# Kernel tuning notes

Measured on AMD Instinct MI355X. Metric: run time of the kernel, lower is better.

Reference implementation:

```python
import jax, jax.numpy as jnp
import numpy as np

EPS = 1e-6
OMEGA = 0.1


def setup_inputs() -> dict:
    key = jax.random.key(0)
    k1, k2 = jax.random.split(key)
    n, d, kk = 4096, 128, 4
    inputs = jax.random.uniform(k1, (n, d), dtype=jnp.float32)  # positive so log(sim) is finite
    labels = jax.random.randint(k2, (n, kk), 0, 64, dtype=jnp.int64)
    return {"inputs": inputs, "labels": labels}


def reference(inputs, labels):
    n, kk = labels.shape
    sim = inputs @ inputs.T                      # [n, n]
    logsim = jnp.log(sim + EPS)                  # a_{jk} = log(sim[j,k]+eps)
    targets = labels[:, 0]
    eye = jnp.eye(n, dtype=bool)
    # pos_mask[j,k] = (targets[j] == targets[k]) xor diagonal
    pos = (targets[:, None] == targets[None, :]) & ~eye
    # eq[j,l,i] = (labels[l,i] == targets[j])
    eq = targets[:, None, None] == labels[None, :, :]
    m_idx = jnp.arange(kk)
    cols = kk - 1 - m_idx                        # neg_mask[m] uses label column kk-1-m
    # neg_mask[m][j,l] == 1  <=>  ~eq[j,l,kk-1-m]  AND  (m==0 or eq[j,l,kk-m])
    neq_col = ~eq[:, :, cols]                    # [j,l,m]
    prev_ok = jnp.concatenate(
        [jnp.ones((n, n, 1), dtype=bool), eq[:, :, cols[:-1]]], axis=-1)
    neg = neq_col & prev_ok                      # [j,l,m]
    # loss_pair[m] = log(Omega+eps) - log(Omega^(kk-m+1)+eps)
    lp = jnp.log(OMEGA + EPS) - jnp.log(OMEGA ** (kk - m_idx + 1) + EPS)  # [kk]
    dt = logsim.dtype
    posf = pos.astype(dt)
    negf = neg.astype(dt)
    # term = (a_jk - b_jlm)^2 with b_jlm = logsim[j,l] + 0.1*lp[m]
    # expand: sum_jklm pos*neg*(a^2 - 2ab + b^2), separable over k and (l,m)
    c = posf.sum(1)                              # [j] count of positives
    S1 = (posf * logsim).sum(1)                  # [j] sum a
    S2 = (posf * logsim ** 2).sum(1)             # [j] sum a^2
    b = logsim[:, :, None] + 0.1 * lp[None, None, :]   # [j,l,m]
    Ncnt = negf.sum(1)                           # [j,m]
    T1 = (negf * b).sum(1)                       # [j,m]
    T2 = (negf * b ** 2).sum(1)                  # [j,m]
    loss = (S2[:, None] * Ncnt - 2.0 * S1[:, None] * T1 + c[:, None] * T2).sum()
    return loss
```

## Files before the change

kernel.cpp:

```cpp
#include <hip/hip_runtime.h>
#include <math.h>

constexpr int N = 4096;
constexpr int D = 128;

constexpr size_t XBF_OFF = 0;
constexpr size_t ACC_OFF = (size_t)1 << 20;
constexpr size_t LSD_OFF = ACC_OFF + 7 * 4096 * 4;
constexpr size_t CNT_OFF = LSD_OFF + 4096 * 4;
constexpr size_t LST_OFF = CNT_OFF + 64 * 32 * 4;
constexpr size_t SUM_OFF = LST_OFF + 64 * 32 * 64 * 2;

typedef __attribute__((ext_vector_type(8))) short short8;
typedef __attribute__((ext_vector_type(4))) float floatx4;
typedef __attribute__((address_space(1))) unsigned int gu32;
typedef __attribute__((address_space(3))) unsigned int lu32;

__device__ inline unsigned f2bf(float f) {
  unsigned u = __builtin_bit_cast(unsigned, f);
  return (u + 0x7FFFu + ((u >> 16) & 1u)) >> 16;
}

__global__ __launch_bounds__(256) void k0_zero(char* __restrict__ ws, float* __restrict__ out) {
  const int idx = blockIdx.x * 256 + threadIdx.x;
  if (idx < 7 * 4096) ((float*)(ws + ACC_OFF))[idx] = 0.f;
  else ((unsigned*)(ws + CNT_OFF))[idx - 7 * 4096] = 0u;
  if (idx == 0) out[0] = 0.f;
}

__global__ __launch_bounds__(256) void k1_prep(
    const float* __restrict__ X, const int* __restrict__ labels, char* __restrict__ ws,
    float B0, float B1, float B2, float B3,
    float Q0, float Q1, float Q2, float Q3) {
  __shared__ float red[4][4];
  const int b = blockIdx.x, tid = threadIdx.x;
  if (b < 64) {
    const int t = b;
    unsigned* cnt = (unsigned*)(ws + CNT_OFF);
    unsigned short* lst = (unsigned short*)(ws + LST_OFF);
    float sg0 = 0.f, sgB = 0.f, sgQ = 0.f, ce0 = 0.f;
    for (int j = tid; j < N; j += 256) {
      const int4 L = ((const int4*)labels)[j];
      const bool e0 = (t == L.x), e1 = (t == L.y), e2 = (t == L.z), e3 = (t == L.w);
      const bool n1 = e3 && !e2, n2 = e2 && !e1, n3 = e1 && !e0;
      sg0 += (e3 ? 0.f : 1.f) + (n1 ? 1.f : 0.f) + (n2 ? 1.f : 0.f) + (n3 ? 1.f : 0.f);
      sgB += (e3 ? 0.f : B0) + (n1 ? B1 : 0.f) + (n2 ? B2 : 0.f) + (n3 ? B3 : 0.f);
      sgQ += (e3 ? 0.f : Q0) + (n1 ? Q1 : 0.f) + (n2 ? Q2 : 0.f) + (n3 ? Q3 : 0.f);
      ce0 += e0 ? 1.f : 0.f;
      const unsigned m = (e0 ? 1u : 0u) | (e1 ? 2u : 0u) | (e2 ? 4u : 0u) | (e3 ? 8u : 0u);
      if (m) {
        const int jb = j >> 7;
        const unsigned slot = atomicAdd(&cnt[t * 32 + jb], 1u);
        if (slot < 64u)
          lst[(t * 32 + jb) * 64 + slot] = (unsigned short)(((j & 127) << 4) | m);
      }
    }
    const int w = tid >> 6, lane = tid & 63;
#pragma unroll
    for (int s = 1; s <= 32; s <<= 1) {
      sg0 += __shfl_xor(sg0, s, 64); sgB += __shfl_xor(sgB, s, 64);
      sgQ += __shfl_xor(sgQ, s, 64); ce0 += __shfl_xor(ce0, s, 64);
    }
    if (lane == 0) { red[w][0] = sg0; red[w][1] = sgB; red[w][2] = sgQ; red[w][3] = ce0; }
    __syncthreads();
    if (tid == 0) {
      float* sums = (float*)(ws + SUM_OFF);
      sums[t * 4 + 0] = red[0][0] + red[1][0] + red[2][0] + red[3][0];
      sums[t * 4 + 1] = red[0][1] + red[1][1] + red[2][1] + red[3][1];
      sums[t * 4 + 2] = red[0][2] + red[1][2] + red[2][2] + red[3][2];
      sums[t * 4 + 3] = red[0][3] + red[1][3] + red[2][3] + red[3][3];
    }
  } else if (b < 320) {
    const int task = (b - 64) * 256 + tid;
    const int r   = task >> 4;
    const int blk = task & 15;
    const float4 x0 = *(const float4*)&X[r * D + blk * 8];
    const float4 x1 = *(const float4*)&X[r * D + blk * 8 + 4];
    uint4 wv;
    wv.x = f2bf(x0.x) | (f2bf(x0.y) << 16);
    wv.y = f2bf(x0.z) | (f2bf(x0.w) << 16);
    wv.z = f2bf(x1.x) | (f2bf(x1.y) << 16);
    wv.w = f2bf(x1.z) | (f2bf(x1.w) << 16);
    *(uint4*)(ws + XBF_OFF + (size_t)r * 256 + ((blk ^ (r & 15)) * 16)) = wv;
  } else {
    const int i = (b - 320) * 256 + tid;
    const float* xr = X + i * D;
    float s = 0.f;
#pragma unroll
    for (int c = 0; c < 32; ++c) {
      const float4 v = ((const float4*)xr)[c];
      s += v.x * v.x + v.y * v.y + v.z * v.z + v.w * v.w;
    }
    ((float*)(ws + LSD_OFF))[i] = __logf(s + 1e-6f);
  }
}

__global__ __launch_bounds__(512, 4) void logratio_phaseA(
    const char* __restrict__ ws_ro, const int* __restrict__ labels,
    float* acc7, float B0, float B1, float B2, float B3) {

  __shared__ __align__(16) char smem[66560];

  const int tid  = threadIdx.x;
  const int w    = tid >> 6;
  const int lane = tid & 63;
  const int lc   = lane & 15;
  const int quad = lane >> 4;
  const int jBase = blockIdx.x * 128;
  const int iBase = blockIdx.y * 128;

  const char* xbf = ws_ro + XBF_OFF;
  const char* gB_ = xbf + (size_t)jBase * 256 + w * 4096 + lane * 16;
  const char* gA_ = xbf + (size_t)iBase * 256 + w * 4096 + lane * 16;
#pragma unroll
  for (int c = 0; c < 4; ++c) {
    __builtin_amdgcn_global_load_lds((const gu32*)(gB_ + c * 1024),
                                     (lu32*)(smem + w * 4096 + c * 1024), 16, 0, 0);
    __builtin_amdgcn_global_load_lds((const gu32*)(gA_ + c * 1024),
                                     (lu32*)(smem + 32768 + w * 4096 + c * 1024), 16, 0, 0);
  }
  __syncthreads();

  floatx4 acc[8] = {};
  const char* Abase = smem + 32768 + (w * 16 + lc) * 256;
#pragma unroll
  for (int kb = 0; kb < 4; ++kb) {
    const int pb = ((kb * 4 + quad) ^ lc) * 16;
    const short8 af = *(const short8*)(Abase + pb);
    short8 bfr[8];
#pragma unroll
    for (int tn = 0; tn < 8; ++tn)
      bfr[tn] = *(const short8*)(smem + (tn * 16 + lc) * 256 + pb);
#pragma unroll
    for (int tn = 0; tn < 8; ++tn)
      acc[tn] = __builtin_amdgcn_mfma_f32_16x16x32_bf16(af, bfr[tn], acc[tn], 0, 0, 0);
  }
  __syncthreads();

  float* lsT   = (float*)smem;
  float* rowTT = (float*)(smem + 65536);

  const int r0 = w * 16 + quad * 4;
  float T0r[4] = {0.f, 0.f, 0.f, 0.f};
  float T1r[4] = {0.f, 0.f, 0.f, 0.f};
#pragma unroll
  for (int tn = 0; tn < 8; ++tn) {
    const int col = tn * 16 + lc;
    floatx4 lsv;
#pragma unroll
    for (int reg = 0; reg < 4; ++reg) {
      const float ls = __logf(acc[tn][reg] + 1e-6f);
      lsv[reg] = ls;
      T0r[reg] += ls;
      T1r[reg] = fmaf(ls, ls, T1r[reg]);
    }
    *(floatx4*)(lsT + col * 128 + (r0 ^ ((col & 7) << 2))) = lsv;
  }
#pragma unroll
  for (int reg = 0; reg < 4; ++reg) {
    float t0 = T0r[reg], t1 = T1r[reg];
#pragma unroll
    for (int s = 1; s <= 8; s <<= 1) {
      t0 += __shfl_xor(t0, s, 64);
      t1 += __shfl_xor(t1, s, 64);
    }
    if (lc == 0) {
      rowTT[(r0 + reg) * 2]     = t0;
      rowTT[(r0 + reg) * 2 + 1] = t1;
    }
  }
  __syncthreads();

  if (tid < 128) {
    const int r = tid, gi = iBase + r;
    const int t = labels[gi * 4];
    const int jb = blockIdx.x;
    const unsigned* cntA = (const unsigned*)(ws_ro + CNT_OFF);
    const unsigned short* lst = (const unsigned short*)(ws_ro + LST_OFF) + (t * 32 + jb) * 64;
    unsigned cnt = cntA[t * 32 + jb];
    if (cnt > 64u) cnt = 64u;
    float U0 = 0.f, U1 = 0.f, V = 0.f, P1 = 0.f, P2 = 0.f;
    for (unsigned k = 0; k < cnt; ++k) {
      const unsigned e = lst[k];
      const int jl = (int)(e >> 4);
      const unsigned m = e & 15u;
      const float ls = lsT[jl * 128 + (r ^ ((jl & 7) << 2))];
      const bool e0 = m & 1u, e1 = m & 2u, e2 = m & 4u, e3 = m & 8u;
      const bool n1 = e3 && !e2, n2 = e2 && !e1, n3 = e1 && !e0;
      const float dg0 = (e3 ? -1.f : 0.f) + (n1 ? 1.f : 0.f) + (n2 ? 1.f : 0.f) + (n3 ? 1.f : 0.f);
      const float dgB = (e3 ? -B0 : 0.f) + (n1 ? B1 : 0.f) + (n2 ? B2 : 0.f) + (n3 ? B3 : 0.f);
      const float e0f = e0 ? 1.f : 0.f;
      U0 = fmaf(dg0, ls, U0);
      U1 = fmaf(dg0 * ls, ls, U1);
      V  = fmaf(dgB, ls, V);
      P1 = fmaf(e0f, ls, P1);
      P2 = fmaf(e0f * ls, ls, P2);
    }
    atomicAdd(&acc7[0 * N + gi], rowTT[r * 2]);
    atomicAdd(&acc7[1 * N + gi], rowTT[r * 2 + 1]);
    atomicAdd(&acc7[2 * N + gi], U0);
    atomicAdd(&acc7[3 * N + gi], U1);
    atomicAdd(&acc7[4 * N + gi], V);
    atomicAdd(&acc7[5 * N + gi], P1);
    atomicAdd(&acc7[6 * N + gi], P2);
  }
}

__global__ __launch_bounds__(256) void logratio_phaseB(
    const char* __restrict__ ws_ro, const int* __restrict__ labels,
    float* out, float B0) {
  const int i = blockIdx.x * 256 + threadIdx.x;
  const float* acc7 = (const float*)(ws_ro + ACC_OFF);
  const float T0 = acc7[0 * N + i], T1 = acc7[1 * N + i];
  const float U0 = acc7[2 * N + i], U1 = acc7[3 * N + i];
  const float V  = acc7[4 * N + i];
  const float P1 = acc7[5 * N + i], P2 = acc7[6 * N + i];
  const int t = labels[i * 4];
  const float4 S = ((const float4*)(ws_ro + SUM_OFF))[t];
  const float lsd = ((const float*)(ws_ro + LSD_OFF))[i];
  const float c  = S.w - 1.f;
  const float S1 = P1 - lsd;
  const float S2 = P2 - lsd * lsd;
  const float A  = S.x;
  const float Bv = T0 + U0 + S.y;
  const float Cv = T1 + U1 + 2.f * fmaf(B0, T0, V) + S.z;
  float v = S2 * A - 2.f * S1 * Bv + c * Cv;
#pragma unroll
  for (int m = 32; m >= 1; m >>= 1) v += __shfl_xor(v, m, 64);
  __shared__ float wsum[4];
  if ((threadIdx.x & 63) == 0) wsum[threadIdx.x >> 6] = v;
  __syncthreads();
  if (threadIdx.x == 0) atomicAdd(out, wsum[0] + wsum[1] + wsum[2] + wsum[3]);
}

extern "C" void kernel_launch(void* const* d_in, const int* in_sizes, int n_in,
                              void* d_out, int out_size, void* d_ws, size_t ws_size,
                              hipStream_t stream) {
  const float* inputs = (const float*)d_in[0];
  const int* labels = (const int*)d_in[1];
  float* out = (float*)d_out;
  char* ws = (char*)d_ws;

  float Bq[4], Qq[4];
  for (int m = 0; m < 4; ++m) {
    const float lpv = logf(0.1f + 1e-6f) - logf(powf(0.1f, (float)(5 - m)) + 1e-6f);
    Bq[m] = 0.1f * lpv;
    Qq[m] = Bq[m] * Bq[m];
  }

  k0_zero<<<120, 256, 0, stream>>>(ws, out);
  k1_prep<<<336, 256, 0, stream>>>(inputs, labels, ws,
                                   Bq[0], Bq[1], Bq[2], Bq[3],
                                   Qq[0], Qq[1], Qq[2], Qq[3]);
  dim3 grid(N / 128, N / 128);
  logratio_phaseA<<<grid, 512, 0, stream>>>(ws, labels, (float*)(ws + ACC_OFF),
                                            Bq[0], Bq[1], Bq[2], Bq[3]);
  logratio_phaseB<<<N / 256, 256, 0, stream>>>(ws, labels, out, Bq[0]);
}
```

Baseline: 97.37 us.

## Group rows by target label and apply dense per-label coefficient tables in GEMM epilogue

The prep kernel now builds, for each target label, a dense per-column coefficient table and a list of the rows carrying that label. It also folds the zeroing kernel into prep. Phase A is launched per (column block, label, chunk). It gathers only rows of that label into LDS and multiplies the logsim tile directly by the table coefficients, replacing the serial sparse list loop and the full row-sum terms. This cuts the serial epilogue, a kernel launch and two atomics per row. In exchange it adds a gather, partially filled tiles, and a hard cap of 128 rows per label.

Result: slower. 112.6 us (+15.6%).

```diff
diff --git a/kernel.cpp b/kernel.cpp
--- a/kernel.cpp
+++ b/kernel.cpp
@@ -5,11 +5,12 @@
 constexpr int D = 128;
 
 constexpr size_t XBF_OFF = 0;
-constexpr size_t ACC_OFF = (size_t)1 << 20;
-constexpr size_t LSD_OFF = ACC_OFF + 7 * 4096 * 4;
-constexpr size_t CNT_OFF = LSD_OFF + 4096 * 4;
-constexpr size_t LST_OFF = CNT_OFF + 64 * 32 * 4;
-constexpr size_t SUM_OFF = LST_OFF + 64 * 32 * 64 * 2;
+constexpr size_t TAB_OFF = (size_t)1 << 20;
+constexpr size_t ACC_OFF = (size_t)5 << 20;
+constexpr size_t LSD_OFF = ACC_OFF + 5 * N * 4;
+constexpr size_t SUM_OFF = LSD_OFF + N * 4;
+constexpr size_t CNT_OFF = SUM_OFF + 64 * 16;
+constexpr size_t PRM_OFF = CNT_OFF + 64 * 4;
 
 typedef __attribute__((ext_vector_type(8))) short short8;
 typedef __attribute__((ext_vector_type(4))) float floatx4;
@@ -21,38 +22,35 @@
   return (u + 0x7FFFu + ((u >> 16) & 1u)) >> 16;
 }
 
-__global__ __launch_bounds__(256) void k0_zero(char* __restrict__ ws, float* __restrict__ out) {
-  const int idx = blockIdx.x * 256 + threadIdx.x;
-  if (idx < 7 * 4096) ((float*)(ws + ACC_OFF))[idx] = 0.f;
-  else ((unsigned*)(ws + CNT_OFF))[idx - 7 * 4096] = 0u;
-  if (idx == 0) out[0] = 0.f;
-}
-
 __global__ __launch_bounds__(256) void k1_prep(
-    const float* __restrict__ X, const int* __restrict__ labels, char* __restrict__ ws,
+    const float* __restrict__ X, const int* __restrict__ labels,
+    char* __restrict__ ws, float* __restrict__ out,
     float B0, float B1, float B2, float B3,
     float Q0, float Q1, float Q2, float Q3) {
-  __shared__ float red[4][4];
   const int b = blockIdx.x, tid = threadIdx.x;
   if (b < 64) {
     const int t = b;
-    unsigned* cnt = (unsigned*)(ws + CNT_OFF);
-    unsigned short* lst = (unsigned short*)(ws + LST_OFF);
+    __shared__ unsigned cursor;
+    __shared__ float red[4][4];
+    if (tid == 0) cursor = 0u;
+    __syncthreads();
+    float4* tab = (float4*)(ws + TAB_OFF) + (size_t)t * N;
+    unsigned short* prm = (unsigned short*)(ws + PRM_OFF) + t * 128;
     float sg0 = 0.f, sgB = 0.f, sgQ = 0.f, ce0 = 0.f;
-    for (int j = tid; j < N; j += 256) {
+#pragma unroll 4
+    for (int k = 0; k < 16; ++k) {
+      const int j = k * 256 + tid;
       const int4 L = ((const int4*)labels)[j];
       const bool e0 = (t == L.x), e1 = (t == L.y), e2 = (t == L.z), e3 = (t == L.w);
       const bool n1 = e3 && !e2, n2 = e2 && !e1, n3 = e1 && !e0;
-      sg0 += (e3 ? 0.f : 1.f) + (n1 ? 1.f : 0.f) + (n2 ? 1.f : 0.f) + (n3 ? 1.f : 0.f);
-      sgB += (e3 ? 0.f : B0) + (n1 ? B1 : 0.f) + (n2 ? B2 : 0.f) + (n3 ? B3 : 0.f);
-      sgQ += (e3 ? 0.f : Q0) + (n1 ? Q1 : 0.f) + (n2 ? Q2 : 0.f) + (n3 ? Q3 : 0.f);
-      ce0 += e0 ? 1.f : 0.f;
-      const unsigned m = (e0 ? 1u : 0u) | (e1 ? 2u : 0u) | (e2 ? 4u : 0u) | (e3 ? 8u : 0u);
-      if (m) {
-        const int jb = j >> 7;
-        const unsigned slot = atomicAdd(&cnt[t * 32 + jb], 1u);
-        if (slot < 64u)
-          lst[(t * 32 + jb) * 64 + slot] = (unsigned short)(((j & 127) << 4) | m);
+      const float g0 = (e3 ? 0.f : 1.f) + (n1 ? 1.f : 0.f) + (n2 ? 1.f : 0.f) + (n3 ? 1.f : 0.f);
+      const float gB = (e3 ? 0.f : B0) + (n1 ? B1 : 0.f) + (n2 ? B2 : 0.f) + (n3 ? B3 : 0.f);
+      const float gQ = (e3 ? 0.f : Q0) + (n1 ? Q1 : 0.f) + (n2 ? Q2 : 0.f) + (n3 ? Q3 : 0.f);
+      tab[j] = make_float4(gB, gQ, g0, e0 ? 1.f : 0.f);
+      sg0 += g0; sgB += gB; sgQ += gQ; ce0 += e0 ? 1.f : 0.f;
+      if (e0) {
+        const unsigned s = atomicAdd(&cursor, 1u);
+        if (s < 128u) prm[s] = (unsigned short)j;
       }
     }
     const int w = tid >> 6, lane = tid & 63;
@@ -69,6 +67,8 @@
       sums[t * 4 + 1] = red[0][1] + red[1][1] + red[2][1] + red[3][1];
       sums[t * 4 + 2] = red[0][2] + red[1][2] + red[2][2] + red[3][2];
       sums[t * 4 + 3] = red[0][3] + red[1][3] + red[2][3] + red[3][3];
+      const unsigned c = cursor;
+      ((unsigned*)(ws + CNT_OFF))[t] = c < 128u ? c : 128u;
     }
   } else if (b < 320) {
     const int task = (b - 64) * 256 + tid;
@@ -82,7 +82,7 @@
     wv.z = f2bf(x1.x) | (f2bf(x1.y) << 16);
     wv.w = f2bf(x1.z) | (f2bf(x1.w) << 16);
     *(uint4*)(ws + XBF_OFF + (size_t)r * 256 + ((blk ^ (r & 15)) * 16)) = wv;
-  } else {
+  } else if (b < 336) {
     const int i = (b - 320) * 256 + tid;
     const float* xr = X + i * D;
     float s = 0.f;
@@ -92,129 +92,127 @@
       s += v.x * v.x + v.y * v.y + v.z * v.z + v.w * v.w;
     }
     ((float*)(ws + LSD_OFF))[i] = __logf(s + 1e-6f);
-  }
-}
-
-__global__ __launch_bounds__(512, 4) void logratio_phaseA(
-    const char* __restrict__ ws_ro, const int* __restrict__ labels,
-    float* acc7, float B0, float B1, float B2, float B3) {
-
-  __shared__ __align__(16) char smem[66560];
-
-  const int tid  = threadIdx.x;
-  const int w    = tid >> 6;
-  const int lane = tid & 63;
-  const int lc   = lane & 15;
-  const int quad = lane >> 4;
-  const int jBase = blockIdx.x * 128;
-  const int iBase = blockIdx.y * 128;
+  } else {
+    const int idx = (b - 336) * 256 + tid;
+    ((float*)(ws + ACC_OFF))[idx] = 0.f;
+    if (idx == 0) out[0] = 0.f;
+  }
+}
+
+__global__ __launch_bounds__(256, 3) void logratio_phaseA(
+    const char* __restrict__ ws_ro, float* acc5) {
+
+  const int jb = blockIdx.x;
+  const int t = blockIdx.y >> 1, chunk = blockIdx.y & 1;
+  const int cnt = (int)((const unsigned*)(ws_ro + CNT_OFF))[t];
+  const int active = min(cnt - chunk * 64, 64);
+  if (active <= 0) return;
+
+  __shared__ __align__(16) char smem[51200];
+  const int tid = threadIdx.x;
+  const int w = tid >> 6, lane = tid & 63;
+  const int lc = lane & 15, quad = lane >> 4;
+  const int jBase = jb * 128;
 
   const char* xbf = ws_ro + XBF_OFF;
-  const char* gB_ = xbf + (size_t)jBase * 256 + w * 4096 + lane * 16;
-  const char* gA_ = xbf + (size_t)iBase * 256 + w * 4096 + lane * 16;
+  {
+    const char* g = xbf + (size_t)jBase * 256 + w * 8192 + lane * 16;
+#pragma unroll
+    for (int c = 0; c < 8; ++c)
+      __builtin_amdgcn_global_load_lds((const gu32*)(g + c * 1024),
+                                       (lu32*)(smem + w * 8192 + c * 1024), 16, 0, 0);
+  }
+  const unsigned short* prm = (const unsigned short*)(ws_ro + PRM_OFF) + t * 128 + chunk * 64;
 #pragma unroll
   for (int c = 0; c < 4; ++c) {
-    __builtin_amdgcn_global_load_lds((const gu32*)(gB_ + c * 1024),
-                                     (lu32*)(smem + w * 4096 + c * 1024), 16, 0, 0);
-    __builtin_amdgcn_global_load_lds((const gu32*)(gA_ + c * 1024),
-                                     (lu32*)(smem + 32768 + w * 4096 + c * 1024), 16, 0, 0);
-  }
-  __syncthreads();
-
+    const int slot = w * 16 + c * 4 + (lane >> 4);
+    const int r = (slot < active) ? (int)prm[slot] : 0;
+    const int p = lane & 15;
+    const char* g = xbf + (size_t)r * 256 + ((p ^ (slot & 15) ^ (r & 15)) * 16);
+    __builtin_amdgcn_global_load_lds((const gu32*)g,
+                                     (lu32*)(smem + 32768 + (w * 16 + c * 4) * 256), 16, 0, 0);
+  }
+  if (w < 2) {
+    const char* g = ws_ro + TAB_OFF + ((size_t)t * N + jBase) * 16 + w * 1024 + lane * 16;
+    __builtin_amdgcn_global_load_lds((const gu32*)g, (lu32*)(smem + 49152 + w * 1024), 16, 0, 0);
+  }
+  __syncthreads();
+
+  const bool act = (w * 16 < active);
   floatx4 acc[8] = {};
-  const char* Abase = smem + 32768 + (w * 16 + lc) * 256;
-#pragma unroll
-  for (int kb = 0; kb < 4; ++kb) {
-    const int pb = ((kb * 4 + quad) ^ lc) * 16;
-    const short8 af = *(const short8*)(Abase + pb);
-    short8 bfr[8];
-#pragma unroll
-    for (int tn = 0; tn < 8; ++tn)
-      bfr[tn] = *(const short8*)(smem + (tn * 16 + lc) * 256 + pb);
-#pragma unroll
-    for (int tn = 0; tn < 8; ++tn)
-      acc[tn] = __builtin_amdgcn_mfma_f32_16x16x32_bf16(af, bfr[tn], acc[tn], 0, 0, 0);
-  }
-  __syncthreads();
-
-  float* lsT   = (float*)smem;
-  float* rowTT = (float*)(smem + 65536);
-
-  const int r0 = w * 16 + quad * 4;
-  float T0r[4] = {0.f, 0.f, 0.f, 0.f};
-  float T1r[4] = {0.f, 0.f, 0.f, 0.f};
-#pragma unroll
-  for (int tn = 0; tn < 8; ++tn) {
-    const int col = tn * 16 + lc;
-    floatx4 lsv;
+  if (act) {
+    const char* Abase = smem + 32768 + (w * 16 + lc) * 256;
+#pragma unroll
+    for (int kb = 0; kb < 4; ++kb) {
+      const int pb = ((kb * 4 + quad) ^ lc) * 16;
+      const short8 af = *(const short8*)(Abase + pb);
+      short8 bfr[8];
+#pragma unroll
+      for (int tn = 0; tn < 8; ++tn)
+        bfr[tn] = *(const short8*)(smem + (tn * 16 + lc) * 256 + pb);
+#pragma unroll
+      for (int tn = 0; tn < 8; ++tn)
+        acc[tn] = __builtin_amdgcn_mfma_f32_16x16x32_bf16(af, bfr[tn], acc[tn], 0, 0, 0);
+    }
+  }
+  __syncthreads();
+  float* Red = (float*)smem;
+
+  if (act) {
+    const float* slice = (const float*)(smem + 49152);
+    float U[4] = {}, W[4] = {}, V[4] = {}, P1[4] = {}, P2[4] = {};
+#pragma unroll
+    for (int tn = 0; tn < 8; ++tn) {
+      const floatx4 cf = *(const floatx4*)(slice + (tn * 16 + lc) * 4);
+      const float gB = cf[0], g0 = cf[2], e0 = cf[3];
+#pragma unroll
+      for (int reg = 0; reg < 4; ++reg) {
+        const float ls = __logf(acc[tn][reg] + 1e-6f);
+        const float u = g0 * ls;
+        U[reg] += u;
+        W[reg] = fmaf(u, ls, W[reg]);
+        V[reg] = fmaf(gB, ls, V[reg]);
+        const float p = e0 * ls;
+        P1[reg] += p;
+        P2[reg] = fmaf(p, ls, P2[reg]);
+      }
+    }
 #pragma unroll
     for (int reg = 0; reg < 4; ++reg) {
-      const float ls = __logf(acc[tn][reg] + 1e-6f);
-      lsv[reg] = ls;
-      T0r[reg] += ls;
-      T1r[reg] = fmaf(ls, ls, T1r[reg]);
-    }
-    *(floatx4*)(lsT + col * 128 + (r0 ^ ((col & 7) << 2))) = lsv;
-  }
-#pragma unroll
-  for (int reg = 0; reg < 4; ++reg) {
-    float t0 = T0r[reg], t1 = T1r[reg];
-#pragma unroll
-    for (int s = 1; s <= 8; s <<= 1) {
-      t0 += __shfl_xor(t0, s, 64);
-      t1 += __shfl_xor(t1, s, 64);
-    }
-    if (lc == 0) {
-      rowTT[(r0 + reg) * 2]     = t0;
-      rowTT[(r0 + reg) * 2 + 1] = t1;
-    }
-  }
-  __syncthreads();
-
-  if (tid < 128) {
-    const int r = tid, gi = iBase + r;
-    const int t = labels[gi * 4];
-    const int jb = blockIdx.x;
-    const unsigned* cntA = (const unsigned*)(ws_ro + CNT_OFF);
-    const unsigned short* lst = (const unsigned short*)(ws_ro + LST_OFF) + (t * 32 + jb) * 64;
-    unsigned cnt = cntA[t * 32 + jb];
-    if (cnt > 64u) cnt = 64u;
-    float U0 = 0.f, U1 = 0.f, V = 0.f, P1 = 0.f, P2 = 0.f;
-    for (unsigned k = 0; k < cnt; ++k) {
-      const unsigned e = lst[k];
-      const int jl = (int)(e >> 4);
-      const unsigned m = e & 15u;
-      const float ls = lsT[jl * 128 + (r ^ ((jl & 7) << 2))];
-      const bool e0 = m & 1u, e1 = m & 2u, e2 = m & 4u, e3 = m & 8u;
-      const bool n1 = e3 && !e2, n2 = e2 && !e1, n3 = e1 && !e0;
-      const float dg0 = (e3 ? -1.f : 0.f) + (n1 ? 1.f : 0.f) + (n2 ? 1.f : 0.f) + (n3 ? 1.f : 0.f);
-      const float dgB = (e3 ? -B0 : 0.f) + (n1 ? B1 : 0.f) + (n2 ? B2 : 0.f) + (n3 ? B3 : 0.f);
-      const float e0f = e0 ? 1.f : 0.f;
-      U0 = fmaf(dg0, ls, U0);
-      U1 = fmaf(dg0 * ls, ls, U1);
-      V  = fmaf(dgB, ls, V);
-      P1 = fmaf(e0f, ls, P1);
-      P2 = fmaf(e0f * ls, ls, P2);
-    }
-    atomicAdd(&acc7[0 * N + gi], rowTT[r * 2]);
-    atomicAdd(&acc7[1 * N + gi], rowTT[r * 2 + 1]);
-    atomicAdd(&acc7[2 * N + gi], U0);
-    atomicAdd(&acc7[3 * N + gi], U1);
-    atomicAdd(&acc7[4 * N + gi], V);
-    atomicAdd(&acc7[5 * N + gi], P1);
-    atomicAdd(&acc7[6 * N + gi], P2);
+      const int row = w * 16 + quad * 4 + reg;
+      float* dst = Red + row * 81 + lc * 5;
+      dst[0] = U[reg]; dst[1] = W[reg]; dst[2] = V[reg]; dst[3] = P1[reg]; dst[4] = P2[reg];
+    }
+  }
+  __syncthreads();
+
+  if (tid < active) {
+    const float* src = Red + tid * 81;
+    float s0 = 0.f, s1 = 0.f, s2 = 0.f, s3 = 0.f, s4 = 0.f;
+#pragma unroll
+    for (int l = 0; l < 16; ++l) {
+      s0 += src[l * 5 + 0]; s1 += src[l * 5 + 1]; s2 += src[l * 5 + 2];
+      s3 += src[l * 5 + 3]; s4 += src[l * 5 + 4];
+    }
+    const int gi = (int)prm[tid];
+    atomicAdd(&acc5[0 * N + gi], s0);
+    atomicAdd(&acc5[1 * N + gi], s1);
+    atomicAdd(&acc5[2 * N + gi], s2);
+    atomicAdd(&acc5[3 * N + gi], s3);
+    atomicAdd(&acc5[4 * N + gi], s4);
   }
 }
 
 __global__ __launch_bounds__(256) void logratio_phaseB(
     const char* __restrict__ ws_ro, const int* __restrict__ labels,
-    float* out, float B0) {
+    float* out) {
   const int i = blockIdx.x * 256 + threadIdx.x;
-  const float* acc7 = (const float*)(ws_ro + ACC_OFF);
-  const float T0 = acc7[0 * N + i], T1 = acc7[1 * N + i];
-  const float U0 = acc7[2 * N + i], U1 = acc7[3 * N + i];
-  const float V  = acc7[4 * N + i];
-  const float P1 = acc7[5 * N + i], P2 = acc7[6 * N + i];
+  const float* acc5 = (const float*)(ws_ro + ACC_OFF);
+  const float U  = acc5[0 * N + i];
+  const float W  = acc5[1 * N + i];
+  const float V  = acc5[2 * N + i];
+  const float P1 = acc5[3 * N + i];
+  const float P2 = acc5[4 * N + i];
   const int t = labels[i * 4];
   const float4 S = ((const float4*)(ws_ro + SUM_OFF))[t];
   const float lsd = ((const float*)(ws_ro + LSD_OFF))[i];
@@ -222,8 +220,8 @@
   const float S1 = P1 - lsd;
   const float S2 = P2 - lsd * lsd;
   const float A  = S.x;
-  const float Bv = T0 + U0 + S.y;
-  const float Cv = T1 + U1 + 2.f * fmaf(B0, T0, V) + S.z;
+  const float Bv = U + S.y;
+  const float Cv = W + 2.f * V + S.z;
   float v = S2 * A - 2.f * S1 * Bv + c * Cv;
 #pragma unroll
   for (int m = 32; m >= 1; m >>= 1) v += __shfl_xor(v, m, 64);
@@ -248,12 +246,10 @@
     Qq[m] = Bq[m] * Bq[m];
   }
 
-  k0_zero<<<120, 256, 0, stream>>>(ws, out);
-  k1_prep<<<336, 256, 0, stream>>>(inputs, labels, ws,
+  k1_prep<<<416, 256, 0, stream>>>(inputs, labels, ws, out,
                                    Bq[0], Bq[1], Bq[2], Bq[3],
                                    Qq[0], Qq[1], Qq[2], Qq[3]);
-  dim3 grid(N / 128, N / 128);
-  logratio_phaseA<<<grid, 512, 0, stream>>>(ws, labels, (float*)(ws + ACC_OFF),
-                                            Bq[0], Bq[1], Bq[2], Bq[3]);
-  logratio_phaseB<<<N / 256, 256, 0, stream>>>(ws, labels, out, Bq[0]);
-}
+  dim3 grid(32, 128);
+  logratio_phaseA<<<grid, 256, 0, stream>>>(ws, (float*)(ws + ACC_OFF));
+  logratio_phaseB<<<N / 256, 256, 0, stream>>>(ws, labels, out);
+}
```
